# Optimization experiments

Measured on AMD Instinct MI355X. Metric: run time of the kernel, lower is better.

The kernel has to match this reference:

```python
import jax, jax.numpy as jnp
import numpy as np


def setup_inputs() -> dict:
    key = jax.random.key(0)
    B, H, N = 1024, 8, 64
    A = jax.random.normal(key, (B, H, N, N), dtype=jnp.float32)
    # Build SPD matrices: P = A A^T / N + eps * I (eigenvalues strictly > 0)
    P = jnp.einsum('bhij,bhkj->bhik', A, A) / N + 1e-3 * jnp.eye(N, dtype=jnp.float32)
    return {"P": P}


def reference(P):
    # LogEig: eigendecompose each SPD matrix, take log of eigenvalues,
    # reconstruct X = U diag(log w) U^T  (batched over [B, H]).
    w, U = jnp.linalg.eigh(P)          # w: [B,H,N], U: [B,H,N,N]
    logw = jnp.log(w)
    return jnp.einsum('bhik,bhk,bhjk->bhij', U, logw, U)
```

## Files before the change

kernel.cpp:

```cpp
#include <hip/hip_runtime.h>
#include <math.h>

#define N 64
#define LDC 68
#define MAX_SWEEPS 10
#define SKIP_TOL2 9e-12f

__device__ __forceinline__ void get_pair(int r, int k, int& p, int& q) {
    if (k == 0) { p = 63; q = r; }
    else {
        p = r + k; if (p >= 63) p -= 63;
        q = r - k; if (q < 0)  q += 63;
    }
}

template <int CTRL>
__device__ __forceinline__ float dpp_add(float x) {
    int m = __builtin_amdgcn_update_dpp(0, __float_as_int(x), CTRL, 0xF, 0xF, true);
    return x + __int_as_float(m);
}

__global__ __launch_bounds__(256)
void logeig_kernel(const float* __restrict__ P, float* __restrict__ Out) {
    __shared__ float As[N * LDC];
    __shared__ float nrm[N];
    __shared__ float lw[N];
    __shared__ int notconv;

    const int t = threadIdx.x;
    const int bid = blockIdx.x;
    const float* A0 = P + (size_t)bid * (N * N);
    float* O = Out + (size_t)bid * (N * N);

    {
        const float4* A4 = (const float4*)A0;
        #pragma unroll
        for (int kk = 0; kk < 4; ++kk) {
            int f = t + kk * 256;
            float4 v = A4[f];
            int e = f << 2;
            int r = e >> 6;
            int i = e & 63;
            *(float4*)&As[r * LDC + i] = v;
        }
    }
    __syncthreads();

    for (int k = 0; k < N; ++k) {
        if (t == 0) As[k * LDC + k] = sqrtf(fmaxf(As[k * LDC + k], 1e-20f));
        __syncthreads();
        {
            float dinv = 1.0f / As[k * LDC + k];
            for (int i = k + 1 + t; i < N; i += 256) As[k * LDC + i] *= dinv;
        }
        __syncthreads();
        for (int j = k + 1 + (t >> 3); j < N; j += 32) {
            float ljk = As[k * LDC + j];
            for (int i = j + (t & 7); i < N; i += 8)
                As[j * LDC + i] = fmaf(-As[k * LDC + i], ljk, As[j * LDC + i]);
        }
        __syncthreads();
    }

    for (int f = t; f < N * N; f += 256) {
        int c = f >> 6, i = f & 63;
        if (i < c) As[c * LDC + i] = 0.f;
    }
    __syncthreads();
    if (t < N) {
        float s = 0.f;
        const float* cc = &As[t * LDC];
        for (int i = 0; i < N; ++i) { float x = cc[i]; s = fmaf(x, x, s); }
        nrm[t] = s;
    }
    __syncthreads();

    const int kp = t >> 3;
    const int g  = t & 7;
    int conv = 0;
    for (int sweep = 0; sweep < MAX_SWEEPS && !conv; ++sweep) {
        if (t == 0) notconv = 0;
        __syncthreads();
        for (int r = 0; r < 63; ++r) {
            int p, q; get_pair(r, kp, p, q);
            float* cp = &As[p * LDC + (g << 3)];
            float* cq = &As[q * LDC + (g << 3)];
            float4 ap0 = *(float4*)cp;
            float4 ap1 = *(float4*)(cp + 4);
            float4 aq0 = *(float4*)cq;
            float4 aq1 = *(float4*)(cq + 4);
            float gd = ap0.x * aq0.x;
            gd = fmaf(ap0.y, aq0.y, gd);
            gd = fmaf(ap0.z, aq0.z, gd);
            gd = fmaf(ap0.w, aq0.w, gd);
            gd = fmaf(ap1.x, aq1.x, gd);
            gd = fmaf(ap1.y, aq1.y, gd);
            gd = fmaf(ap1.z, aq1.z, gd);
            gd = fmaf(ap1.w, aq1.w, gd);
            gd = dpp_add<0xB1>(gd);
            gd = dpp_add<0x4E>(gd);
            gd = dpp_add<0x141>(gd);
            float a = nrm[p], b = nrm[q];
            if (gd * gd > SKIP_TOL2 * a * b) {
                float tau = (b - a) / (2.f * gd);
                float tt = 1.f / (fabsf(tau) + sqrtf(fmaf(tau, tau, 1.f)));
                if (tau < 0.f) tt = -tt;
                float c = rsqrtf(fmaf(tt, tt, 1.f));
                float s = tt * c;
                float4 np0, np1, nq0, nq1;
                np0.x = c * ap0.x - s * aq0.x;  nq0.x = s * ap0.x + c * aq0.x;
                np0.y = c * ap0.y - s * aq0.y;  nq0.y = s * ap0.y + c * aq0.y;
                np0.z = c * ap0.z - s * aq0.z;  nq0.z = s * ap0.z + c * aq0.z;
                np0.w = c * ap0.w - s * aq0.w;  nq0.w = s * ap0.w + c * aq0.w;
                np1.x = c * ap1.x - s * aq1.x;  nq1.x = s * ap1.x + c * aq1.x;
                np1.y = c * ap1.y - s * aq1.y;  nq1.y = s * ap1.y + c * aq1.y;
                np1.z = c * ap1.z - s * aq1.z;  nq1.z = s * ap1.z + c * aq1.z;
                np1.w = c * ap1.w - s * aq1.w;  nq1.w = s * ap1.w + c * aq1.w;
                *(float4*)cp = np0;
                *(float4*)(cp + 4) = np1;
                *(float4*)cq = nq0;
                *(float4*)(cq + 4) = nq1;
                if (g == 0) {
                    nrm[p] = a - tt * gd;
                    nrm[q] = b + tt * gd;
                    notconv = 1;
                }
            }
            __syncthreads();
        }
        conv = (notconv == 0);
        __syncthreads();
    }

    if (t < N) {
        float s = 0.f;
        const float* cc = &As[t * LDC];
        for (int i = 0; i < N; ++i) { float x = cc[i]; s = fmaf(x, x, s); }
        s = fmaxf(s, 1e-30f);
        lw[t] = logf(s) / s;
    }
    __syncthreads();

    {
        int ti = t >> 4;
        int tj = t & 15;
        float acc[4][4];
        #pragma unroll
        for (int a2 = 0; a2 < 4; ++a2)
            #pragma unroll
            for (int b2 = 0; b2 < 4; ++b2) acc[a2][b2] = 0.f;

        for (int k = 0; k < N; ++k) {
            float w = lw[k];
            float4 ui = *(const float4*)&As[k * LDC + 4 * ti];
            float4 uj = *(const float4*)&As[k * LDC + 4 * tj];
            uj.x *= w; uj.y *= w; uj.z *= w; uj.w *= w;
            float ua[4] = {ui.x, ui.y, ui.z, ui.w};
            float ub[4] = {uj.x, uj.y, uj.z, uj.w};
            #pragma unroll
            for (int a2 = 0; a2 < 4; ++a2)
                #pragma unroll
                for (int b2 = 0; b2 < 4; ++b2)
                    acc[a2][b2] = fmaf(ua[a2], ub[b2], acc[a2][b2]);
        }
        #pragma unroll
        for (int a2 = 0; a2 < 4; ++a2) {
            float4 vout = make_float4(acc[a2][0], acc[a2][1], acc[a2][2], acc[a2][3]);
            ((float4*)O)[(4 * ti + a2) * 16 + tj] = vout;
        }
    }
}

extern "C" void kernel_launch(void* const* d_in, const int* in_sizes, int n_in,
                              void* d_out, int out_size, void* d_ws, size_t ws_size,
                              hipStream_t stream) {
    const float* P = (const float*)d_in[0];
    float* Out = (float*)d_out;
    int nmat = in_sizes[0] / (N * N);
    logeig_kernel<<<dim3(nmat), dim3(256), 0, stream>>>(P, Out);
}
```

Baseline: 3.025 ms.

## Streamline Jacobi sweep: incremental pairing, double-buffered convergence flag, fast intrinsics

Replaces the per-round pair computation with incremental p/q updates and changes each thread's column slice from 8 contiguous floats to two strided float4 chunks, which should reduce LDS bank conflicts. A double-buffered convergence flag removes one barrier per sweep. The Cholesky step uses a single rsqrt instead of a separate serial sqrt and barrier, and the rotation and log math use raw AMD rcp/sqrt/rsq/log intrinsics. The approximate intrinsics trade some precision for fewer instructions.

After: 3.033 ms. Within noise of the previous version (+0.3%).

```diff
diff --git a/kernel.cpp b/kernel.cpp
--- a/kernel.cpp
+++ b/kernel.cpp
@@ -6,13 +6,10 @@
 #define MAX_SWEEPS 10
 #define SKIP_TOL2 9e-12f
 
-__device__ __forceinline__ void get_pair(int r, int k, int& p, int& q) {
-    if (k == 0) { p = 63; q = r; }
-    else {
-        p = r + k; if (p >= 63) p -= 63;
-        q = r - k; if (q < 0)  q += 63;
-    }
-}
+__device__ __forceinline__ float frcp(float x)   { return __builtin_amdgcn_rcpf(x); }
+__device__ __forceinline__ float fsqrt_(float x) { return __builtin_amdgcn_sqrtf(x); }
+__device__ __forceinline__ float frsq(float x)   { return __builtin_amdgcn_rsqf(x); }
+__device__ __forceinline__ float flog_(float x)  { return __builtin_amdgcn_logf(x) * 0.69314718056f; }
 
 template <int CTRL>
 __device__ __forceinline__ float dpp_add(float x) {
@@ -25,7 +22,7 @@
     __shared__ float As[N * LDC];
     __shared__ float nrm[N];
     __shared__ float lw[N];
-    __shared__ int notconv;
+    __shared__ int ncv[2];
 
     const int t = threadIdx.x;
     const int bid = blockIdx.x;
@@ -47,12 +44,10 @@
     __syncthreads();
 
     for (int k = 0; k < N; ++k) {
-        if (t == 0) As[k * LDC + k] = sqrtf(fmaxf(As[k * LDC + k], 1e-20f));
-        __syncthreads();
-        {
-            float dinv = 1.0f / As[k * LDC + k];
-            for (int i = k + 1 + t; i < N; i += 256) As[k * LDC + i] *= dinv;
-        }
+        float dval = fmaxf(As[k * LDC + k], 1e-20f);
+        float dinv = frsq(dval);
+        for (int i = k + 1 + t; i < N; i += 256) As[k * LDC + i] *= dinv;
+        if (t == 0) As[k * LDC + k] = dval * dinv;
         __syncthreads();
         for (int j = k + 1 + (t >> 3); j < N; j += 32) {
             float ljk = As[k * LDC + j];
@@ -66,6 +61,7 @@
         int c = f >> 6, i = f & 63;
         if (i < c) As[c * LDC + i] = 0.f;
     }
+    if (t == 0) { ncv[0] = 0; ncv[1] = 0; }
     __syncthreads();
     if (t < N) {
         float s = 0.f;
@@ -77,18 +73,22 @@
 
     const int kp = t >> 3;
     const int g  = t & 7;
+    float* colg = As + 4 * g;
+
+    int p, q;
+    if (kp == 0) { p = 63; q = 0; } else { p = kp; q = 63 - kp; }
+    unsigned rotated = 0;
     int conv = 0;
+
     for (int sweep = 0; sweep < MAX_SWEEPS && !conv; ++sweep) {
-        if (t == 0) notconv = 0;
-        __syncthreads();
         for (int r = 0; r < 63; ++r) {
-            int p, q; get_pair(r, kp, p, q);
-            float* cp = &As[p * LDC + (g << 3)];
-            float* cq = &As[q * LDC + (g << 3)];
+            float* cp = colg + p * LDC;
+            float* cq = colg + q * LDC;
             float4 ap0 = *(float4*)cp;
-            float4 ap1 = *(float4*)(cp + 4);
+            float4 ap1 = *(float4*)(cp + 32);
             float4 aq0 = *(float4*)cq;
-            float4 aq1 = *(float4*)(cq + 4);
+            float4 aq1 = *(float4*)(cq + 32);
+            float a = nrm[p], b = nrm[q];
             float gd = ap0.x * aq0.x;
             gd = fmaf(ap0.y, aq0.y, gd);
             gd = fmaf(ap0.z, aq0.z, gd);
@@ -100,12 +100,11 @@
             gd = dpp_add<0xB1>(gd);
             gd = dpp_add<0x4E>(gd);
             gd = dpp_add<0x141>(gd);
-            float a = nrm[p], b = nrm[q];
             if (gd * gd > SKIP_TOL2 * a * b) {
-                float tau = (b - a) / (2.f * gd);
-                float tt = 1.f / (fabsf(tau) + sqrtf(fmaf(tau, tau, 1.f)));
+                float tau = (b - a) * 0.5f * frcp(gd);
+                float tt = frcp(fabsf(tau) + fsqrt_(fmaf(tau, tau, 1.f)));
                 if (tau < 0.f) tt = -tt;
-                float c = rsqrtf(fmaf(tt, tt, 1.f));
+                float c = frsq(fmaf(tt, tt, 1.f));
                 float s = tt * c;
                 float4 np0, np1, nq0, nq1;
                 np0.x = c * ap0.x - s * aq0.x;  nq0.x = s * ap0.x + c * aq0.x;
@@ -117,19 +116,24 @@
                 np1.z = c * ap1.z - s * aq1.z;  nq1.z = s * ap1.z + c * aq1.z;
                 np1.w = c * ap1.w - s * aq1.w;  nq1.w = s * ap1.w + c * aq1.w;
                 *(float4*)cp = np0;
-                *(float4*)(cp + 4) = np1;
+                *(float4*)(cp + 32) = np1;
                 *(float4*)cq = nq0;
-                *(float4*)(cq + 4) = nq1;
+                *(float4*)(cq + 32) = nq1;
                 if (g == 0) {
                     nrm[p] = a - tt * gd;
                     nrm[q] = b + tt * gd;
-                    notconv = 1;
                 }
+                rotated = 1;
             }
             __syncthreads();
+            q = (q == 62) ? 0 : q + 1;
+            if (kp) p = (p == 62) ? 0 : p + 1;
         }
-        conv = (notconv == 0);
+        if (rotated) ncv[sweep & 1] = 1;
+        if (t == 0) ncv[(sweep & 1) ^ 1] = 0;
+        rotated = 0;
         __syncthreads();
+        conv = (ncv[sweep & 1] == 0);
     }
 
     if (t < N) {
@@ -137,7 +141,7 @@
         const float* cc = &As[t * LDC];
         for (int i = 0; i < N; ++i) { float x = cc[i]; s = fmaf(x, x, s); }
         s = fmaxf(s, 1e-30f);
-        lw[t] = logf(s) / s;
+        lw[t] = flog_(s) * frcp(s);
     }
     __syncthreads();
 
```
